# Kernel tuning notes

Measured on AMD Instinct MI355X. Metric: run time of the kernel, lower is better.

## Reference

```python
import jax, jax.numpy as jnp
import numpy as np

Z_DIM = 32
POLY_ORDER = 3
INCLUDE_BIAS = True

# Static index arrays replicating the nested-loop term ordering of the torch code.
_I2, _J2 = np.triu_indices(Z_DIM)  # pairs (i, j) with i <= j, row-major in i -> matches loop order
_TRIPLES = np.array([(i, j, k) for i in range(Z_DIM) for j in range(i, Z_DIM) for k in range(j, Z_DIM)], dtype=np.int32)
_TI, _TJ, _TK = _TRIPLES[:, 0], _TRIPLES[:, 1], _TRIPLES[:, 2]


def build_library(z):
    # z: [B, d] -> Theta: [B, n_terms], same column order as build_library_torch
    B = z.shape[0]
    terms = []
    if INCLUDE_BIAS:
        terms.append(jnp.ones((B, 1), dtype=z.dtype))
    terms.append(z)
    if POLY_ORDER >= 2:
        terms.append(z[:, _I2] * z[:, _J2])  # [B, C(d+1,2)] quadratic terms
    if POLY_ORDER >= 3:
        terms.append(z[:, _TI] * z[:, _TJ] * z[:, _TK])  # [B, C(d+2,3)] cubic terms
    return jnp.concatenate(terms, axis=1)


def setup_inputs() -> dict:
    key = jax.random.key(0)
    k1, k2 = jax.random.split(key)
    B = 65536
    n_terms = 6545  # 1 + 32 + 528 + 5984 for d=32, order=3, bias
    z = jax.random.normal(k1, (B, Z_DIM), dtype=jnp.float32)
    Xi = jax.random.normal(k2, (n_terms, Z_DIM), dtype=jnp.float32)
    Xi_mask = jnp.ones((n_terms, Z_DIM), dtype=jnp.float32)
    z_mean = jnp.zeros((1, Z_DIM), dtype=jnp.float32)
    z_std = jnp.ones((1, Z_DIM), dtype=jnp.float32)
    return {"z": z, "Xi": Xi, "Xi_mask": Xi_mask, "z_mean": z_mean, "z_std": z_std}


def reference(z, Xi, Xi_mask, z_mean, z_std):
    # NOTE: the original module computes z_norm = (z - z_mean) / z_std but
    # never uses it; Theta is built from the raw z. Reproduce exactly.
    Theta = build_library(z)            # [B, n_terms]
    Xi_eff = Xi * Xi_mask               # [n_terms, z_dim]
    dz_dt = Theta @ Xi_eff              # [B, z_dim]
    return dz_dt
```

## Files before the change

### kernel.cpp

```cpp
#include <hip/hip_runtime.h>


#define Z 32
#define ROWS 65536
#define NBLK (ROWS / 64)

#define NCHUNK 552
#define NGRAN (NCHUNK * 2)
#define NGP 1120
#define KSPAN 138

typedef short short8 __attribute__((ext_vector_type(8)));
typedef float f32x16 __attribute__((ext_vector_type(16)));
typedef float float2v __attribute__((ext_vector_type(2)));

struct Sched {
    unsigned mg[NGP];
    short rt[NGRAN * 8];
    int nq[4];
};

constexpr Sched make_sched() {
    Sched s{};
    short gi[NGP] = {}, gj[NGP] = {};
    char gt[NGP] = {}, gq[NGP] = {};
    int tidx[32][32] = {}, pidx[32] = {};
    {
        int n = 0;
        for (int a = 0; a < 32; ++a)
            for (int b = a; b < 32; ++b) { tidx[a][b] = n; n += 32 - b; }
        for (int i = 0; i < 32; ++i) pidx[i] = i * 32 - i * (i - 1) / 2;
    }
    int g = 0;
    for (int q = 0; q < 4; ++q) {
        int g0 = g;
        for (int b = 0; b < 32; ++b)
            if ((b >> 3) <= q)
                for (int a = 0; a <= b; ++a) { gi[g]=(short)a; gj[g]=(short)b; gt[g]=0; gq[g]=(char)q; ++g; }
        for (int b = 0; b < 32; ++b)
            if ((b >> 3) >= q) { gi[g]=(short)b; gj[g]=32; gt[g]=1; gq[g]=(char)q; ++g; }
        gi[g]=32; gj[g]=32; gt[g]=2; gq[g]=(char)q; ++g;
        while ((g - g0) & 7) { gi[g]=32; gj[g]=32; gt[g]=3; gq[g]=(char)q; ++g; }
        s.nq[q] = (g - g0) / 2;
    }
    for (int gg = 0; gg < NGRAN; ++gg) {
        s.mg[gg] = ((unsigned)gi[gg] * 256u) | (((unsigned)gj[gg] * 256u) << 16);
        int i = gi[gg], j = gj[gg], ty = gt[gg], q = gq[gg];
        for (int jj = 0; jj < 8; ++jj) {
            int k = 8 * q + jj, row = -1;
            if (ty == 0)      { if (k >= j) row = 561 + tidx[i][j] + (k - j); }
            else if (ty == 1) { if (k <= i) row = 33 + pidx[k] + (i - k); }
            else if (ty == 2) { row = 1 + k; }
            s.rt[gg * 8 + jj] = (short)row;
        }
    }
    return s;
}
constexpr Sched S = make_sched();
static_assert(S.nq[0] == 36 && S.nq[1] == 84 && S.nq[2] == 160 && S.nq[3] == 272, "chunk counts");

__device__ __forceinline__ unsigned pack_bf16(float s0, float s1) {
    return __builtin_amdgcn_perm(__builtin_bit_cast(unsigned, s1),
                                 __builtin_bit_cast(unsigned, s0), 0x07060302u);
}

__device__ __forceinline__ void dma16(const uint4* g, uint4* lds_lane) {
    __builtin_amdgcn_global_load_lds(
        (const __attribute__((address_space(1))) unsigned*)g,
        (__attribute__((address_space(3))) unsigned*)lds_lane, 16, 0, 0);
}

__device__ __forceinline__ void wait_vm0() {
    asm volatile("s_waitcnt vmcnt(0)" ::: "memory");
}

__global__ void sindy_prep(const float* __restrict__ Xi,
                           const float* __restrict__ Xi_mask,
                           uint2* __restrict__ Bp2, size_t ws_size) {
    __shared__ unsigned short sh[8][32];
    const int tid = threadIdx.x;
    const int jj = tid >> 5, n = tid & 31;
#pragma unroll
    for (int pass = 0; pass < 4; ++pass) {
        int g = blockIdx.x * 4 + pass;
        int row = S.rt[g * 8 + jj];
        float f = 0.0f;
        if (row >= 0) f = Xi[row * Z + n] * Xi_mask[row * Z + n];
        unsigned u = __builtin_bit_cast(unsigned, f);
        sh[jj][n] = (unsigned short)((u + 0x7FFFu + ((u >> 16) & 1u)) >> 16);
        __syncthreads();
        if (tid < 64) {
            int n2 = tid & 31, rep = tid >> 5;
            unsigned v0 = sh[4*rep+0][n2], v1 = sh[4*rep+1][n2];
            unsigned v2 = sh[4*rep+2][n2], v3 = sh[4*rep+3][n2];
            int c = g >> 1, h = g & 1;
            size_t idx = ((size_t)c * 64 + h * 32 + n2) * 2 + rep;
            if ((idx + 1) * 8 <= ws_size)
                Bp2[idx] = uint2{v0 | (v1 << 16), v2 | (v3 << 16)};
        }
        __syncthreads();
    }
}

__global__ __launch_bounds__(256, 4) void sindy_mfma(const float* __restrict__ z,
                                                     const float* __restrict__ Xi,
                                                     const float* __restrict__ Xi_mask,
                                                     const uint4* __restrict__ Bp,
                                                     float* __restrict__ out) {
    const int lane = threadIdx.x & 63;
    const int kh = threadIdx.x >> 6;
    const int m = lane & 31;
    const int half = lane >> 5;
    const long R = (long)blockIdx.x * 64;

    __shared__ float zs[33][2][32];
    __shared__ float cs[2][32][32];
    __shared__ unsigned mg_sh[NGP];
    __shared__ uint4 bring[4][4][64];

    for (int t = threadIdx.x; t < NGP; t += 256) mg_sh[t] = S.mg[t];
    for (int idx = threadIdx.x; idx < 512; idx += 256) {
        int row = idx >> 3, q4 = idx & 7;
        float4 v = ((const float4*)(z + (R + row) * Z))[q4];
        int t = row >> 5, mm = row & 31;
        zs[4*q4+0][t][mm] = v.x; zs[4*q4+1][t][mm] = v.y;
        zs[4*q4+2][t][mm] = v.z; zs[4*q4+3][t][mm] = v.w;
    }
    if (threadIdx.x < 64) zs[32][threadIdx.x >> 5][threadIdx.x & 31] = 1.0f;
    __syncthreads();

    const int c0 = kh * KSPAN;
    const char* zmb = (const char*)&zs[0][0][0] + 4 * m;
    const unsigned* mgh = mg_sh + half;
    const uint4* bpl = Bp + lane;

    dma16(bpl + (size_t)(c0+0) * 64, &bring[kh][(c0+0) & 3][lane]);
    dma16(bpl + (size_t)(c0+1) * 64, &bring[kh][(c0+1) & 3][lane]);
    wait_vm0();

    unsigned u0 = mgh[2*c0], u1 = mgh[2*c0+2];
    float pA0, pA1, pB0, pB1;
    {
        float i0 = *(const float*)(zmb + (u0 & 0xFFFFu)), i1 = *(const float*)(zmb + (u0 & 0xFFFFu) + 128);
        float j0 = *(const float*)(zmb + (u0 >> 16)),     j1 = *(const float*)(zmb + (u0 >> 16) + 128);
        pA0 = i0 * j0; pA1 = i1 * j1;
        float e0 = *(const float*)(zmb + (u1 & 0xFFFFu)), e1 = *(const float*)(zmb + (u1 & 0xFFFFu) + 128);
        float f0 = *(const float*)(zmb + (u1 >> 16)),     f1 = *(const float*)(zmb + (u1 >> 16) + 128);
        pB0 = e0 * f0; pB1 = e1 * f1;
    }
    unsigned w0s = mgh[2*c0+4], w1s = mgh[2*c0+6];

    f32x16 acc0 = {}, acc1 = {};

    auto seg = [&](int Q, int cbeg, int cfin) {
        const char* zq = zmb + Q * 2048;
        float2v zA0, zA1, zA2, zA3, zB0, zB1, zB2, zB3;
        zA0.x = *(const float*)(zq +    0); zB0.x = *(const float*)(zq +  128);
        zA0.y = *(const float*)(zq +  256); zB0.y = *(const float*)(zq +  384);
        zA1.x = *(const float*)(zq +  512); zB1.x = *(const float*)(zq +  640);
        zA1.y = *(const float*)(zq +  768); zB1.y = *(const float*)(zq +  896);
        zA2.x = *(const float*)(zq + 1024); zB2.x = *(const float*)(zq + 1152);
        zA2.y = *(const float*)(zq + 1280); zB2.y = *(const float*)(zq + 1408);
        zA3.x = *(const float*)(zq + 1536); zB3.x = *(const float*)(zq + 1664);
        zA3.y = *(const float*)(zq + 1792); zB3.y = *(const float*)(zq + 1920);

        auto mfma0 = [&](float pp, const uint4& bv) {
            float2v p2; p2.x = pp; p2.y = pp;
            union { unsigned u[4]; short8 sv; } a;
            float2v t0 = p2 * zA0; a.u[0] = pack_bf16(t0.x, t0.y);
            float2v t1 = p2 * zA1; a.u[1] = pack_bf16(t1.x, t1.y);
            float2v t2 = p2 * zA2; a.u[2] = pack_bf16(t2.x, t2.y);
            float2v t3 = p2 * zA3; a.u[3] = pack_bf16(t3.x, t3.y);
            union { uint4 v; short8 sv; } b; b.v = bv;
            acc0 = __builtin_amdgcn_mfma_f32_32x32x16_bf16(a.sv, b.sv, acc0, 0, 0, 0);
        };
        auto mfma1 = [&](float pp, const uint4& bv) {
            float2v p2; p2.x = pp; p2.y = pp;
            union { unsigned u[4]; short8 sv; } a;
            float2v t0 = p2 * zB0; a.u[0] = pack_bf16(t0.x, t0.y);
            float2v t1 = p2 * zB1; a.u[1] = pack_bf16(t1.x, t1.y);
            float2v t2 = p2 * zB2; a.u[2] = pack_bf16(t2.x, t2.y);
            float2v t3 = p2 * zB3; a.u[3] = pack_bf16(t3.x, t3.y);
            union { uint4 v; short8 sv; } b; b.v = bv;
            acc1 = __builtin_amdgcn_mfma_f32_32x32x16_bf16(a.sv, b.sv, acc1, 0, 0, 0);
        };

        for (int c = cbeg; c < cfin; c += 2) {
            int l2 = c + 2, l3 = c + 3;
            int s2 = l2 < NCHUNK ? l2 : NCHUNK - 1;
            int s3 = l3 < NCHUNK ? l3 : NCHUNK - 1;
            dma16(bpl + (size_t)s2 * 64, &bring[kh][l2 & 3][lane]);
            dma16(bpl + (size_t)s3 * 64, &bring[kh][l3 & 3][lane]);
            uint4 bA = bring[kh][c & 3][lane];
            uint4 bB = bring[kh][(c + 1) & 3][lane];
            unsigned nw0 = mgh[2*c+8], nw1 = mgh[2*c+10];
            float a0i = *(const float*)(zmb + (w0s & 0xFFFFu));
            float a1i = *(const float*)(zmb + (w0s & 0xFFFFu) + 128);
            float a0j = *(const float*)(zmb + (w0s >> 16));
            float a1j = *(const float*)(zmb + (w0s >> 16) + 128);
            float b0i = *(const float*)(zmb + (w1s & 0xFFFFu));
            float b1i = *(const float*)(zmb + (w1s & 0xFFFFu) + 128);
            float b0j = *(const float*)(zmb + (w1s >> 16));
            float b1j = *(const float*)(zmb + (w1s >> 16) + 128);
            mfma0(pA0, bA); mfma1(pA1, bA);
            mfma0(pB0, bB); mfma1(pB1, bB);
            pA0 = a0i * a0j; pA1 = a1i * a1j; pB0 = b0i * b0j; pB1 = b1i * b1j;
            w0s = nw0; w1s = nw1;
            wait_vm0();
        }
    };

    if (kh == 0)      { seg(0,   0,  36); seg(1,  36, 120); seg(2, 120, 138); }
    else if (kh == 1) { seg(2, 138, 276); }
    else if (kh == 2) { seg(2, 276, 280); seg(3, 280, 414); }
    else              { seg(3, 414, 552); }

    if (kh == 3) {
#pragma unroll
        for (int r = 0; r < 16; ++r) {
            int row = (r & 3) + 8 * (r >> 2) + 4 * half;
            cs[0][row][m] = acc0[r]; cs[1][row][m] = acc1[r];
        }
    }
    __syncthreads();
    if (kh == 2) {
#pragma unroll
        for (int r = 0; r < 16; ++r) {
            int row = (r & 3) + 8 * (r >> 2) + 4 * half;
            cs[0][row][m] += acc0[r]; cs[1][row][m] += acc1[r];
        }
    }
    __syncthreads();
    if (kh == 1) {
#pragma unroll
        for (int r = 0; r < 16; ++r) {
            int row = (r & 3) + 8 * (r >> 2) + 4 * half;
            cs[0][row][m] += acc0[r]; cs[1][row][m] += acc1[r];
        }
    }
    __syncthreads();
    if (kh == 0) {
        const float bias = Xi[m] * Xi_mask[m];
        float* o0 = out + R * Z;
        float* o1 = out + (R + 32) * Z;
#pragma unroll
        for (int r = 0; r < 16; ++r) {
            int row = (r & 3) + 8 * (r >> 2) + 4 * half;
            o0[row * Z + m] = acc0[r] + cs[0][row][m] + bias;
            o1[row * Z + m] = acc1[r] + cs[1][row][m] + bias;
        }
    }
}

extern "C" void kernel_launch(void* const* d_in, const int* in_sizes, int n_in,
                              void* d_out, int out_size, void* d_ws, size_t ws_size,
                              hipStream_t stream) {
    const float* z       = (const float*)d_in[0];
    const float* Xi      = (const float*)d_in[1];
    const float* Xi_mask = (const float*)d_in[2];
    float* out = (float*)d_out;
    uint4* Bp  = (uint4*)d_ws;

    sindy_prep<<<NGRAN / 4, 256, 0, stream>>>(Xi, Xi_mask, (uint2*)d_ws, ws_size);
    sindy_mfma<<<NBLK, 256, 0, stream>>>(z, Xi, Xi_mask, Bp, out);
}
```

Measured before the change: 119.9 us.

## Switch MFMA operands from bf16 to fp16 and prefetch B into registers

Replaces the bf16 packing path (fp32 multiply then perm-based truncation) with fp16 operands. The z values are converted once per segment with cvt_pkrtz, and the A-fragment products are formed with packed half multiplies before an f16 MFMA. The prep kernel now writes Xi as fp16 instead of rounded bf16. Separately, the global-to-LDS DMA ring with explicit vmcnt waits is replaced by a plain register double-buffer of B fragments loaded from global memory. The aim is to cut VALU work per MFMA and drop the LDS ring and full waits, at the risk of fp16 range and overflow issues for cubic products and the compiler inserting its own waits.

```diff
diff --git a/kernel.cpp b/kernel.cpp
--- a/kernel.cpp
+++ b/kernel.cpp
@@ -10,9 +10,13 @@
 #define NGP 1120
 #define KSPAN 138
 
-typedef short short8 __attribute__((ext_vector_type(8)));
 typedef float f32x16 __attribute__((ext_vector_type(16)));
-typedef float float2v __attribute__((ext_vector_type(2)));
+typedef _Float16 h2 __attribute__((ext_vector_type(2)));
+typedef _Float16 h8 __attribute__((ext_vector_type(8)));
+
+__device__ __forceinline__ h2 pkrtz(float a, float b) {
+    return __builtin_bit_cast(h2, __builtin_amdgcn_cvt_pkrtz(a, b));
+}
 
 struct Sched {
     unsigned mg[NGP];
@@ -59,21 +63,6 @@
 constexpr Sched S = make_sched();
 static_assert(S.nq[0] == 36 && S.nq[1] == 84 && S.nq[2] == 160 && S.nq[3] == 272, "chunk counts");
 
-__device__ __forceinline__ unsigned pack_bf16(float s0, float s1) {
-    return __builtin_amdgcn_perm(__builtin_bit_cast(unsigned, s1),
-                                 __builtin_bit_cast(unsigned, s0), 0x07060302u);
-}
-
-__device__ __forceinline__ void dma16(const uint4* g, uint4* lds_lane) {
-    __builtin_amdgcn_global_load_lds(
-        (const __attribute__((address_space(1))) unsigned*)g,
-        (__attribute__((address_space(3))) unsigned*)lds_lane, 16, 0, 0);
-}
-
-__device__ __forceinline__ void wait_vm0() {
-    asm volatile("s_waitcnt vmcnt(0)" ::: "memory");
-}
-
 __global__ void sindy_prep(const float* __restrict__ Xi,
                            const float* __restrict__ Xi_mask,
                            uint2* __restrict__ Bp2, size_t ws_size) {
@@ -86,8 +75,8 @@
         int row = S.rt[g * 8 + jj];
         float f = 0.0f;
         if (row >= 0) f = Xi[row * Z + n] * Xi_mask[row * Z + n];
-        unsigned u = __builtin_bit_cast(unsigned, f);
-        sh[jj][n] = (unsigned short)((u + 0x7FFFu + ((u >> 16) & 1u)) >> 16);
+        _Float16 hh = (_Float16)f;
+        sh[jj][n] = __builtin_bit_cast(unsigned short, hh);
         __syncthreads();
         if (tid < 64) {
             int n2 = tid & 31, rep = tid >> 5;
@@ -116,7 +105,6 @@
     __shared__ float zs[33][2][32];
     __shared__ float cs[2][32][32];
     __shared__ unsigned mg_sh[NGP];
-    __shared__ uint4 bring[4][4][64];
 
     for (int t = threadIdx.x; t < NGP; t += 256) mg_sh[t] = S.mg[t];
     for (int idx = threadIdx.x; idx < 512; idx += 256) {
@@ -134,9 +122,8 @@
     const unsigned* mgh = mg_sh + half;
     const uint4* bpl = Bp + lane;
 
-    dma16(bpl + (size_t)(c0+0) * 64, &bring[kh][(c0+0) & 3][lane]);
-    dma16(bpl + (size_t)(c0+1) * 64, &bring[kh][(c0+1) & 3][lane]);
-    wait_vm0();
+    uint4 bufA = bpl[(size_t)(c0 + 0) * 64];
+    uint4 bufB = bpl[(size_t)(c0 + 1) * 64];
 
     unsigned u0 = mgh[2*c0], u1 = mgh[2*c0+2];
     float pA0, pA1, pB0, pB1;
@@ -154,45 +141,45 @@
 
     auto seg = [&](int Q, int cbeg, int cfin) {
         const char* zq = zmb + Q * 2048;
-        float2v zA0, zA1, zA2, zA3, zB0, zB1, zB2, zB3;
-        zA0.x = *(const float*)(zq +    0); zB0.x = *(const float*)(zq +  128);
-        zA0.y = *(const float*)(zq +  256); zB0.y = *(const float*)(zq +  384);
-        zA1.x = *(const float*)(zq +  512); zB1.x = *(const float*)(zq +  640);
-        zA1.y = *(const float*)(zq +  768); zB1.y = *(const float*)(zq +  896);
-        zA2.x = *(const float*)(zq + 1024); zB2.x = *(const float*)(zq + 1152);
-        zA2.y = *(const float*)(zq + 1280); zB2.y = *(const float*)(zq + 1408);
-        zA3.x = *(const float*)(zq + 1536); zB3.x = *(const float*)(zq + 1664);
-        zA3.y = *(const float*)(zq + 1792); zB3.y = *(const float*)(zq + 1920);
+        h2 zA0, zA1, zA2, zA3, zB0, zB1, zB2, zB3;
+        {
+            float a0 = *(const float*)(zq +    0), a1 = *(const float*)(zq +  256);
+            float a2 = *(const float*)(zq +  512), a3 = *(const float*)(zq +  768);
+            float a4 = *(const float*)(zq + 1024), a5 = *(const float*)(zq + 1280);
+            float a6 = *(const float*)(zq + 1536), a7 = *(const float*)(zq + 1792);
+            float b0 = *(const float*)(zq +  128), b1 = *(const float*)(zq +  384);
+            float b2 = *(const float*)(zq +  640), b3 = *(const float*)(zq +  896);
+            float b4 = *(const float*)(zq + 1152), b5 = *(const float*)(zq + 1408);
+            float b6 = *(const float*)(zq + 1664), b7 = *(const float*)(zq + 1920);
+            zA0 = pkrtz(a0, a1); zA1 = pkrtz(a2, a3);
+            zA2 = pkrtz(a4, a5); zA3 = pkrtz(a6, a7);
+            zB0 = pkrtz(b0, b1); zB1 = pkrtz(b2, b3);
+            zB2 = pkrtz(b4, b5); zB3 = pkrtz(b6, b7);
+        }
 
         auto mfma0 = [&](float pp, const uint4& bv) {
-            float2v p2; p2.x = pp; p2.y = pp;
-            union { unsigned u[4]; short8 sv; } a;
-            float2v t0 = p2 * zA0; a.u[0] = pack_bf16(t0.x, t0.y);
-            float2v t1 = p2 * zA1; a.u[1] = pack_bf16(t1.x, t1.y);
-            float2v t2 = p2 * zA2; a.u[2] = pack_bf16(t2.x, t2.y);
-            float2v t3 = p2 * zA3; a.u[3] = pack_bf16(t3.x, t3.y);
-            union { uint4 v; short8 sv; } b; b.v = bv;
-            acc0 = __builtin_amdgcn_mfma_f32_32x32x16_bf16(a.sv, b.sv, acc0, 0, 0, 0);
+            h2 p2 = pkrtz(pp, pp);
+            union { h2 h[4]; h8 v; } a;
+            a.h[0] = p2 * zA0; a.h[1] = p2 * zA1;
+            a.h[2] = p2 * zA2; a.h[3] = p2 * zA3;
+            union { uint4 v; h8 h; } b; b.v = bv;
+            acc0 = __builtin_amdgcn_mfma_f32_32x32x16_f16(a.v, b.h, acc0, 0, 0, 0);
         };
         auto mfma1 = [&](float pp, const uint4& bv) {
-            float2v p2; p2.x = pp; p2.y = pp;
-            union { unsigned u[4]; short8 sv; } a;
-            float2v t0 = p2 * zB0; a.u[0] = pack_bf16(t0.x, t0.y);
-            float2v t1 = p2 * zB1; a.u[1] = pack_bf16(t1.x, t1.y);
-            float2v t2 = p2 * zB2; a.u[2] = pack_bf16(t2.x, t2.y);
-            float2v t3 = p2 * zB3; a.u[3] = pack_bf16(t3.x, t3.y);
-            union { uint4 v; short8 sv; } b; b.v = bv;
-            acc1 = __builtin_amdgcn_mfma_f32_32x32x16_bf16(a.sv, b.sv, acc1, 0, 0, 0);
+            h2 p2 = pkrtz(pp, pp);
+            union { h2 h[4]; h8 v; } a;
+            a.h[0] = p2 * zB0; a.h[1] = p2 * zB1;
+            a.h[2] = p2 * zB2; a.h[3] = p2 * zB3;
+            union { uint4 v; h8 h; } b; b.v = bv;
+            acc1 = __builtin_amdgcn_mfma_f32_32x32x16_f16(a.v, b.h, acc1, 0, 0, 0);
         };
 
         for (int c = cbeg; c < cfin; c += 2) {
             int l2 = c + 2, l3 = c + 3;
             int s2 = l2 < NCHUNK ? l2 : NCHUNK - 1;
             int s3 = l3 < NCHUNK ? l3 : NCHUNK - 1;
-            dma16(bpl + (size_t)s2 * 64, &bring[kh][l2 & 3][lane]);
-            dma16(bpl + (size_t)s3 * 64, &bring[kh][l3 & 3][lane]);
-            uint4 bA = bring[kh][c & 3][lane];
-            uint4 bB = bring[kh][(c + 1) & 3][lane];
+            uint4 nA = bpl[(size_t)s2 * 64];
+            uint4 nB = bpl[(size_t)s3 * 64];
             unsigned nw0 = mgh[2*c+8], nw1 = mgh[2*c+10];
             float a0i = *(const float*)(zmb + (w0s & 0xFFFFu));
             float a1i = *(const float*)(zmb + (w0s & 0xFFFFu) + 128);
@@ -202,11 +189,11 @@
             float b1i = *(const float*)(zmb + (w1s & 0xFFFFu) + 128);
             float b0j = *(const float*)(zmb + (w1s >> 16));
             float b1j = *(const float*)(zmb + (w1s >> 16) + 128);
-            mfma0(pA0, bA); mfma1(pA1, bA);
-            mfma0(pB0, bB); mfma1(pB1, bB);
+            mfma0(pA0, bufA); mfma1(pA1, bufA);
+            mfma0(pB0, bufB); mfma1(pB1, bufB);
             pA0 = a0i * a0j; pA1 = a1i * a1j; pB0 = b0i * b0j; pB1 = b1i * b1j;
             w0s = nw0; w1s = nw1;
-            wait_vm0();
+            bufA = nA; bufB = nB;
         }
     };
 
```

New measurement: 112.4 us. 1.07x faster.
